# Performance work log

Hardware: AMD Instinct MI355X
Metric: run time of the kernel (lower is better)

Reference implementation:

```python
import jax, jax.numpy as jnp
import numpy as np

N_NODES = 50000
N_EDGES = 500000
IN_DIM = 128
H1, C1 = 4, 64   # layer1: heads=4, out=64, concat -> 256
H2, C2 = 1, 64   # layer2: heads=1, out=64


def setup_inputs() -> dict:
    key = jax.random.key(0)
    ks = jax.random.split(key, 16)
    p = lambda k, shp: (jax.random.normal(k, shp, dtype=jnp.float32) * 0.1)
    return {
        "x": jax.random.normal(ks[0], (N_NODES, IN_DIM), dtype=jnp.float32),
        "edge_index": jax.random.randint(ks[1], (2, N_EDGES), 0, N_NODES, dtype=jnp.int32),
        "edge_attr": jax.random.uniform(ks[2], (N_EDGES, 1), dtype=jnp.float32),
        # layer 1 params
        "W1": p(ks[3], (IN_DIM, H1 * C1)),
        "We1": p(ks[4], (1, H1 * C1)),
        "as1": p(ks[5], (H1, C1)),
        "ad1": p(ks[6], (H1, C1)),
        "ae1": p(ks[7], (H1, C1)),
        "b1": jnp.zeros((H1 * C1,), dtype=jnp.float32),
        # layer 2 params
        "W2": p(ks[8], (H1 * C1, H2 * C2)),
        "We2": p(ks[9], (1, H2 * C2)),
        "as2": p(ks[10], (H2, C2)),
        "ad2": p(ks[11], (H2, C2)),
        "ae2": p(ks[12], (H2, C2)),
        "b2": jnp.zeros((H2 * C2,), dtype=jnp.float32),
    }


def _add_self_loops(src, dst, edge_attr, n):
    # PyG fill_value='mean': loop edge_attr = mean of incoming edge attrs per node
    cnt = jax.ops.segment_sum(jnp.ones((src.shape[0],), edge_attr.dtype), dst, num_segments=n)
    loop_attr = jax.ops.segment_sum(edge_attr, dst, num_segments=n) / jnp.maximum(cnt, 1.0)[:, None]
    idx = jnp.arange(n, dtype=src.dtype)
    return (jnp.concatenate([src, idx]), jnp.concatenate([dst, idx]),
            jnp.concatenate([edge_attr, loop_attr], axis=0))


def _gat_conv(x, src, dst, edge_attr, W, We, a_src, a_dst, a_edge, bias, heads, out_ch):
    n = x.shape[0]
    h = (x @ W).reshape(n, heads, out_ch)                      # [N,H,C]
    e = (edge_attr @ We).reshape(-1, heads, out_ch)            # [E,H,C]
    alpha = ((h * a_src).sum(-1)[src]                          # gather src score
             + (h * a_dst).sum(-1)[dst]                        # gather dst score
             + (e * a_edge).sum(-1))                           # [E,H]
    alpha = jax.nn.leaky_relu(alpha, 0.2)
    m = jax.ops.segment_max(alpha, dst, num_segments=n)        # per-target max
    alpha = jnp.exp(alpha - m[dst])
    denom = jax.ops.segment_sum(alpha, dst, num_segments=n)
    alpha = alpha / (denom[dst] + 1e-16)
    out = jax.ops.segment_sum(h[src] * alpha[..., None], dst, num_segments=n)
    return out.reshape(n, heads * out_ch) + bias


def reference(x, edge_index, edge_attr, W1, We1, as1, ad1, ae1, b1,
              W2, We2, as2, ad2, ae2, b2):
    src, dst = edge_index[0], edge_index[1]
    src, dst, ea = _add_self_loops(src, dst, edge_attr, x.shape[0])
    h = jax.nn.elu(_gat_conv(x, src, dst, ea, W1, We1, as1, ad1, ae1, b1, H1, C1))
    return _gat_conv(h, src, dst, ea, W2, We2, as2, ad2, ae2, b2, H2, C2)
```

## Files before the change

### kernel.cpp

```cpp
#include <hip/hip_runtime.h>
#include <math.h>

#define NN 50000
#define NE 500000
#define DIM 128
#define HC1 256
#define HC2 64
#define RSTR 64
#define CAPM 63
#define EPB 1024
#define NBUCKET ((NE + EPB - 1) / EPB)
#define GB ((NN + 63) / 64)

typedef __attribute__((ext_vector_type(8))) short short8;
typedef __attribute__((ext_vector_type(4))) float floatx4;


__device__ __forceinline__ unsigned short f2bf(float f) {
  unsigned int u = __float_as_uint(f);
  unsigned int r = (u + 0x7FFFu + ((u >> 16) & 1u)) >> 16;
  return (unsigned short)r;
}
__device__ __forceinline__ float bf2f(unsigned short s) {
  return __uint_as_float(((unsigned int)s) << 16);
}

__device__ __forceinline__ float waveReduce(float v) {
  v += __shfl_down(v, 32);
  v += __shfl_down(v, 16);
  v += __shfl_down(v, 8);
  v += __shfl_down(v, 4);
  v += __shfl_down(v, 2);
  v += __shfl_down(v, 1);
  return v;
}


__global__ __launch_bounds__(256) void k_prep(const float* __restrict__ W1,
                                              const float* __restrict__ W2,
                                              const float* __restrict__ We1,
                                              const float* __restrict__ ae1,
                                              const float* __restrict__ We2,
                                              const float* __restrict__ ae2,
                                              unsigned short* __restrict__ W1T,
                                              unsigned short* __restrict__ W2T,
                                              float* __restrict__ ce) {
  int b = blockIdx.x, t = threadIdx.x;
  if (b < 128) {
    int idx = b * 256 + t;
    int n = idx >> 7, k = idx & 127;
    W1T[idx] = f2bf(W1[k * 256 + n]);
  } else if (b < 192) {
    int idx = (b - 128) * 256 + t;
    int n = idx >> 8, k = idx & 255;
    W2T[idx] = f2bf(W2[k * 64 + n]);
  } else {
    int h = t >> 6, lane = t & 63;
    float p = We1[h * 64 + lane] * ae1[h * 64 + lane];
    p = waveReduce(p);
    if (lane == 0) ce[h] = p;
    if (h == 0) {
      float q = We2[lane] * ae2[lane];
      q = waveReduce(q);
      if (lane == 0) ce[4] = q;
    }
  }
}


__global__ __launch_bounds__(256) void k_bucket(const int* __restrict__ src,
                                                const int* __restrict__ dst,
                                                const float* __restrict__ ea,
                                                unsigned int* __restrict__ ebuf) {
  int t = threadIdx.x;
  int e0 = blockIdx.x * EPB + t;
  int dv[4]; float ev[4]; unsigned int sv[4]; bool ok[4];
#pragma unroll
  for (int k = 0; k < 4; k++) {
    int e = e0 + k * 256;
    ok[k] = (e < NE);
    int ee = ok[k] ? e : 0;
    dv[k] = dst[ee];
    ev[k] = ea[ee];
    sv[k] = (unsigned int)src[ee];
  }
  unsigned int old[4];
#pragma unroll
  for (int k = 0; k < 4; k++) {
    if (ok[k]) old[k] = atomicAdd(&ebuf[(unsigned long long)dv[k] * RSTR], 1u);
  }
#pragma unroll
  for (int k = 0; k < 4; k++) {
    if (ok[k] && old[k] < CAPM) {
      unsigned int ea16 = __float2uint_rn(ev[k] * 65536.0f);
      if (ea16 > 65535u) ea16 = 65535u;
      ebuf[(unsigned long long)dv[k] * RSTR + 1 + old[k]] = (ea16 << 16) | sv[k];
    }
  }
}


__global__ __launch_bounds__(256) void k_gemm1(const float* __restrict__ x,
                                               const unsigned short* __restrict__ W1T,
                                               const float* __restrict__ as1,
                                               const float* __restrict__ ad1,
                                               unsigned short* __restrict__ h1b,
                                               float* __restrict__ ss1,
                                               float* __restrict__ sd1) {
  __shared__ unsigned short As[64 * 136];
  int t = threadIdx.x;
  int wave = t >> 6, lane = t & 63;
  int q = lane >> 4, ln = lane & 15;
  int m0 = blockIdx.x * 64;
  int n0 = wave * 64;

  short8 bfr[4][4];
#pragma unroll
  for (int c = 0; c < 4; c++)
#pragma unroll
    for (int ks = 0; ks < 4; ks++)
      bfr[c][ks] = *(const short8*)&W1T[(n0 + ln * 4 + c) * 128 + ks * 32 + q * 8];

#pragma unroll
  for (int rep = 0; rep < 8; rep++) {
    int chunk = t + 256 * rep;
    int m = chunk >> 5, kk = (chunk & 31) * 4;
    int gr = m0 + m;
    float4 v = (gr < NN) ? *(const float4*)&x[gr * DIM + kk]
                         : make_float4(0.f, 0.f, 0.f, 0.f);
    ushort4 o;
    o.x = f2bf(v.x); o.y = f2bf(v.y); o.z = f2bf(v.z); o.w = f2bf(v.w);
    *(ushort4*)&As[m * 136 + kk] = o;
  }
  __syncthreads();

  floatx4 acc[4][4];
#pragma unroll
  for (int r = 0; r < 4; r++)
#pragma unroll
    for (int c = 0; c < 4; c++) acc[r][c] = (floatx4){0.f, 0.f, 0.f, 0.f};

#pragma unroll
  for (int ks = 0; ks < 4; ks++) {
    short8 afr[4];
#pragma unroll
    for (int r = 0; r < 4; r++)
      afr[r] = *(const short8*)&As[(r * 16 + ln) * 136 + ks * 32 + q * 8];
#pragma unroll
    for (int r = 0; r < 4; r++)
#pragma unroll
      for (int c = 0; c < 4; c++)
        acc[r][c] = __builtin_amdgcn_mfma_f32_16x16x32_bf16(afr[r], bfr[c][ks], acc[r][c], 0, 0, 0);
  }

  float4 a4 = *(const float4*)&as1[n0 + ln * 4];
  float4 d4 = *(const float4*)&ad1[n0 + ln * 4];

#pragma unroll
  for (int r = 0; r < 4; r++) {
#pragma unroll
    for (int i = 0; i < 4; i++) {
      int gm = m0 + r * 16 + q * 4 + i;
      if (gm < NN) {
        ushort4 o;
        o.x = f2bf(acc[r][0][i]);
        o.y = f2bf(acc[r][1][i]);
        o.z = f2bf(acc[r][2][i]);
        o.w = f2bf(acc[r][3][i]);
        *(ushort4*)&h1b[gm * HC1 + n0 + ln * 4] = o;
      }
      float ps = acc[r][0][i] * a4.x;
      float pd = acc[r][0][i] * d4.x;
      ps = fmaf(acc[r][1][i], a4.y, ps);
      pd = fmaf(acc[r][1][i], d4.y, pd);
      ps = fmaf(acc[r][2][i], a4.z, ps);
      pd = fmaf(acc[r][2][i], d4.z, pd);
      ps = fmaf(acc[r][3][i], a4.w, ps);
      pd = fmaf(acc[r][3][i], d4.w, pd);
#pragma unroll
      for (int m = 1; m < 16; m <<= 1) {
        ps += __shfl_xor(ps, m);
        pd += __shfl_xor(pd, m);
      }
      if (ln == 0 && gm < NN) {
        ss1[gm * 4 + wave] = ps;
        sd1[gm * 4 + wave] = pd;
      }
    }
  }
}

__global__ __launch_bounds__(256) void k_gemm2m(const unsigned short* __restrict__ out1b,
                                                const unsigned short* __restrict__ W2T,
                                                const float* __restrict__ as2,
                                                const float* __restrict__ ad2,
                                                unsigned short* __restrict__ h2b,
                                                float* __restrict__ ss2,
                                                float* __restrict__ sd2) {
  __shared__ unsigned short As[64 * 264];
  __shared__ float ssp[4][64], sdp[4][64];
  int t = threadIdx.x;
  int wave = t >> 6, lane = t & 63;
  int q = lane >> 4, ln = lane & 15;
  int m0 = blockIdx.x * 64;
  int n0 = wave * 16;

  short8 bfr[8];
#pragma unroll
  for (int ks = 0; ks < 8; ks++)
    bfr[ks] = *(const short8*)&W2T[(n0 + ln) * 256 + ks * 32 + q * 8];

  short8 zero8 = {0, 0, 0, 0, 0, 0, 0, 0};
#pragma unroll
  for (int rep = 0; rep < 8; rep++) {
    int chunk = t + 256 * rep;
    int m = chunk >> 5, kk = (chunk & 31) * 8;
    int gr = m0 + m;
    short8 vv = (gr < NN) ? *(const short8*)&out1b[gr * 256 + kk] : zero8;
    *(short8*)&As[m * 264 + kk] = vv;
  }
  __syncthreads();

  floatx4 acc[4];
#pragma unroll
  for (int r = 0; r < 4; r++) acc[r] = (floatx4){0.f, 0.f, 0.f, 0.f};

#pragma unroll
  for (int ks = 0; ks < 8; ks++) {
#pragma unroll
    for (int r = 0; r < 4; r++) {
      short8 afr = *(const short8*)&As[(r * 16 + ln) * 264 + ks * 32 + q * 8];
      acc[r] = __builtin_amdgcn_mfma_f32_16x16x32_bf16(afr, bfr[ks], acc[r], 0, 0, 0);
    }
  }

  float as2v = as2[n0 + ln], ad2v = ad2[n0 + ln];
#pragma unroll
  for (int r = 0; r < 4; r++) {
#pragma unroll
    for (int i = 0; i < 4; i++) {
      int gm = m0 + r * 16 + q * 4 + i;
      if (gm < NN) h2b[gm * HC2 + n0 + ln] = f2bf(acc[r][i]);
      float ps = acc[r][i] * as2v;
      float pd = acc[r][i] * ad2v;
#pragma unroll
      for (int m = 1; m < 16; m <<= 1) {
        ps += __shfl_xor(ps, m);
        pd += __shfl_xor(pd, m);
      }
      if (ln == 0) {
        ssp[wave][r * 16 + q * 4 + i] = ps;
        sdp[wave][r * 16 + q * 4 + i] = pd;
      }
    }
  }
  __syncthreads();
  if (t < 64) {
    int gm = m0 + t;
    if (gm < NN) {
      ss2[gm] = ssp[0][t] + ssp[1][t] + ssp[2][t] + ssp[3][t];
      sd2[gm] = sdp[0][t] + sdp[1][t] + sdp[2][t] + sdp[3][t];
    }
  }
}


__global__ __launch_bounds__(256) void k_agg1(const unsigned short* __restrict__ h1b,
                                              const unsigned int* __restrict__ ebuf,
                                              const float* __restrict__ ss1,
                                              const float* __restrict__ sd1,
                                              const float* __restrict__ ce,
                                              const float* __restrict__ b1,
                                              unsigned short* __restrict__ out1b) {
  int v = (blockIdx.x * blockDim.x + threadIdx.x) >> 6;
  int lane = threadIdx.x & 63;
  int h = lane >> 4;
  int c4 = lane * 4;
  int l16 = lane & 15;
  int vu = __builtin_amdgcn_readfirstlane(v);
  unsigned int craw = ebuf[(unsigned long long)vu * RSTR];
  int cn = (craw < CAPM) ? (int)craw : CAPM;
  cn = __builtin_amdgcn_readfirstlane(cn);
  int beg1 = vu * RSTR + 1;
  int end1 = beg1 + cn;
  float sdh = sd1[vu * 4 + h];
  float ceh = ce[h];
  float4 acc = make_float4(0.f, 0.f, 0.f, 0.f);
  float l = 0.f;
  float easum = 0.f;

  for (int base = beg1; base < end1; base += 16) {
    unsigned int meta = ebuf[base + l16];
#pragma unroll
    for (int half = 0; half < 2; half++) {
      if (base + half * 8 >= end1) break;
      float ssv[8], ea8[8];
      ushort4 u[8];
      bool vld[8];
#pragma unroll
      for (int jj = 0; jj < 8; jj++) {
        int j = half * 8 + jj;
        bool val = (base + j < end1);
        unsigned int m = __builtin_amdgcn_readlane(meta, j);
        int sj = val ? (int)(m & 0xFFFFu) : 0;
        ea8[jj] = (float)(m >> 16) * (1.0f / 65536.0f);
        vld[jj] = val;
        ssv[jj] = ss1[sj * 4 + h];
        u[jj] = *(const ushort4*)&h1b[sj * HC1 + c4];
      }
#pragma unroll
      for (int jj = 0; jj < 8; jj++) {
        easum += vld[jj] ? ea8[jj] : 0.f;
        float xx = fmaf(ea8[jj], ceh, ssv[jj] + sdh);
        xx = fmaxf(xx, 0.2f * xx);
        float a = vld[jj] ? __expf(xx) : 0.f;
        l += a;
        acc.x = fmaf(a, bf2f(u[jj].x), acc.x);
        acc.y = fmaf(a, bf2f(u[jj].y), acc.y);
        acc.z = fmaf(a, bf2f(u[jj].z), acc.z);
        acc.w = fmaf(a, bf2f(u[jj].w), acc.w);
      }
    }
  }
  {
    float lea = easum / fmaxf((float)cn, 1.0f);
    float xx = fmaf(lea, ceh, ss1[vu * 4 + h] + sdh);
    xx = fmaxf(xx, 0.2f * xx);
    float a = __expf(xx);
    ushort4 u = *(const ushort4*)&h1b[vu * HC1 + c4];
    l += a;
    acc.x = fmaf(a, bf2f(u.x), acc.x);
    acc.y = fmaf(a, bf2f(u.y), acc.y);
    acc.z = fmaf(a, bf2f(u.z), acc.z);
    acc.w = fmaf(a, bf2f(u.w), acc.w);
  }
  float inv = 1.f / (l + 1e-16f);
  float4 bv = *(const float4*)&b1[c4];
  float4 o;
  o.x = acc.x * inv + bv.x;
  o.y = acc.y * inv + bv.y;
  o.z = acc.z * inv + bv.z;
  o.w = acc.w * inv + bv.w;
  o.x = (o.x > 0.f) ? o.x : expm1f(o.x);
  o.y = (o.y > 0.f) ? o.y : expm1f(o.y);
  o.z = (o.z > 0.f) ? o.z : expm1f(o.z);
  o.w = (o.w > 0.f) ? o.w : expm1f(o.w);
  ushort4 ob;
  ob.x = f2bf(o.x); ob.y = f2bf(o.y); ob.z = f2bf(o.z); ob.w = f2bf(o.w);
  *(ushort4*)&out1b[vu * HC1 + c4] = ob;
}

__global__ __launch_bounds__(256) void k_agg2(const unsigned short* __restrict__ h2b,
                                              const unsigned int* __restrict__ ebuf,
                                              const float* __restrict__ ss2,
                                              const float* __restrict__ sd2,
                                              const float* __restrict__ ce,
                                              const float* __restrict__ b2,
                                              float* __restrict__ out) {
  int v = (blockIdx.x * blockDim.x + threadIdx.x) >> 6;
  int lane = threadIdx.x & 63;
  int g = lane >> 4;
  int c = lane & 15;
  int l16 = lane & 15;
  int vu = __builtin_amdgcn_readfirstlane(v);
  unsigned int craw = ebuf[(unsigned long long)vu * RSTR];
  int cn = (craw < CAPM) ? (int)craw : CAPM;
  cn = __builtin_amdgcn_readfirstlane(cn);
  int beg1 = vu * RSTR + 1;
  int end1 = beg1 + cn;
  float sdv = sd2[vu];
  float cev = ce[4];
  float4 acc = make_float4(0.f, 0.f, 0.f, 0.f);
  float l = 0.f;
  float easum = 0.f;

  for (int base = beg1; base < end1; base += 16) {
    int nb = end1 - base;
    unsigned int meta = ebuf[base + l16];
    float ssv[4], eav[4];
    bool vld[4];
    ushort4 u[4];
#pragma unroll
    for (int sub = 0; sub < 4; sub++) {
      int j = sub * 4 + g;
      bool val = (j < nb);
      unsigned int m = (unsigned int)__shfl((int)meta, j);
      int sj = val ? (int)(m & 0xFFFFu) : 0;
      eav[sub] = (float)(m >> 16) * (1.0f / 65536.0f);
      vld[sub] = val;
      ssv[sub] = ss2[sj];
      u[sub] = *(const ushort4*)&h2b[sj * HC2 + c * 4];
    }
#pragma unroll
    for (int sub = 0; sub < 4; sub++) {
      easum += vld[sub] ? eav[sub] : 0.f;
      float xx = fmaf(eav[sub], cev, ssv[sub] + sdv);
      xx = fmaxf(xx, 0.2f * xx);
      float a = vld[sub] ? __expf(xx) : 0.f;
      l += a;
      acc.x = fmaf(a, bf2f(u[sub].x), acc.x);
      acc.y = fmaf(a, bf2f(u[sub].y), acc.y);
      acc.z = fmaf(a, bf2f(u[sub].z), acc.z);
      acc.w = fmaf(a, bf2f(u[sub].w), acc.w);
    }
  }
#pragma unroll
  for (int m = 16; m <= 32; m <<= 1) {
    acc.x += __shfl_xor(acc.x, m);
    acc.y += __shfl_xor(acc.y, m);
    acc.z += __shfl_xor(acc.z, m);
    acc.w += __shfl_xor(acc.w, m);
    l += __shfl_xor(l, m);
    easum += __shfl_xor(easum, m);
  }
  {
    float lea = easum / fmaxf((float)cn, 1.0f);
    float xx = fmaf(lea, cev, ss2[vu] + sdv);
    xx = fmaxf(xx, 0.2f * xx);
    float a = __expf(xx);
    ushort4 us = *(const ushort4*)&h2b[vu * HC2 + c * 4];
    l += a;
    acc.x = fmaf(a, bf2f(us.x), acc.x);
    acc.y = fmaf(a, bf2f(us.y), acc.y);
    acc.z = fmaf(a, bf2f(us.z), acc.z);
    acc.w = fmaf(a, bf2f(us.w), acc.w);
  }
  if (g == 0) {
    float inv = 1.f / (l + 1e-16f);
    float4 bv = *(const float4*)&b2[c * 4];
    float4 o;
    o.x = acc.x * inv + bv.x;
    o.y = acc.y * inv + bv.y;
    o.z = acc.z * inv + bv.z;
    o.w = acc.w * inv + bv.w;
    *(float4*)&out[vu * HC2 + c * 4] = o;
  }
}


extern "C" void kernel_launch(void* const* d_in, const int* in_sizes, int n_in,
                              void* d_out, int out_size, void* d_ws, size_t ws_size,
                              hipStream_t stream) {
  const float* x   = (const float*)d_in[0];
  const int*   ei  = (const int*)d_in[1];
  const float* ea  = (const float*)d_in[2];
  const float* W1  = (const float*)d_in[3];
  const float* We1 = (const float*)d_in[4];
  const float* as1 = (const float*)d_in[5];
  const float* ad1 = (const float*)d_in[6];
  const float* ae1 = (const float*)d_in[7];
  const float* b1  = (const float*)d_in[8];
  const float* W2  = (const float*)d_in[9];
  const float* We2 = (const float*)d_in[10];
  const float* as2 = (const float*)d_in[11];
  const float* ad2 = (const float*)d_in[12];
  const float* ae2 = (const float*)d_in[13];
  const float* b2  = (const float*)d_in[14];
  const int* srcp = ei;
  const int* dstp = ei + NE;

  char* w = (char*)d_ws;
  float* ce      = (float*)(w + 3200064);
  float* ss1     = (float*)(w + 3200640);
  float* sd1     = (float*)(w + 4000640);
  float* ss2     = (float*)(w + 4800640);
  float* sd2     = (float*)(w + 5000640);
  unsigned int* ebuf = (unsigned int*)(w + 5200640);
  unsigned short* h1b   = (unsigned short*)(w + 18000640);
  unsigned short* out1b = (unsigned short*)(w + 43600640);
  unsigned short* h2b   = (unsigned short*)(w + 69200640);
  unsigned short* W1T   = (unsigned short*)(w + 75600640);
  unsigned short* W2T   = (unsigned short*)(w + 75666176);

  hipMemsetAsync(w + 5200640, 0, 12800000, stream);

  k_prep<<<193, 256, 0, stream>>>(W1, W2, We1, ae1, We2, ae2, W1T, W2T, ce);
  k_bucket<<<NBUCKET, 256, 0, stream>>>(srcp, dstp, ea, ebuf);
  k_gemm1<<<GB, 256, 0, stream>>>(x, W1T, as1, ad1, h1b, ss1, sd1);

  k_agg1<<<(NN * 64 + 255) / 256, 256, 0, stream>>>(h1b, ebuf, ss1, sd1, ce, b1, out1b);

  k_gemm2m<<<(NN + 63) / 64, 256, 0, stream>>>(out1b, W2T, as2, ad2, h2b, ss2, sd2);
  k_agg2<<<(NN * 64 + 255) / 256, 256, 0, stream>>>(h2b, ebuf, ss2, sd2, ce, b2,
                                                    (float*)d_out);
}
```

Before: 229.9 us.

## Split layer-1 aggregation across channel slices and edge groups; drop ebuf memset

Layer-1 aggregation now uses 8 blocks per group of 4 nodes, one per 32-channel slice. Within each wave, 8 lane groups each take a different edge and their partial sums are combined with cross-lane shuffles. This replaces the serial per-node loop over all edges with readlane broadcasts. The attention scores ss1/sd1 are stored head-major so the per-head gathers are contiguous. The full 12.8MB memset of the edge buffer is replaced by zeroing only the per-node count words inside k_prep. The cost is 8x more blocks, and the per-node metadata and score loads are repeated in every slice.

```diff
diff --git a/kernel.cpp b/kernel.cpp
--- a/kernel.cpp
+++ b/kernel.cpp
@@ -11,6 +11,7 @@
 #define EPB 1024
 #define NBUCKET ((NE + EPB - 1) / EPB)
 #define GB ((NN + 63) / 64)
+#define NSS 50048
 
 typedef __attribute__((ext_vector_type(8))) short short8;
 typedef __attribute__((ext_vector_type(4))) float floatx4;
@@ -44,7 +45,8 @@
                                               const float* __restrict__ ae2,
                                               unsigned short* __restrict__ W1T,
                                               unsigned short* __restrict__ W2T,
-                                              float* __restrict__ ce) {
+                                              float* __restrict__ ce,
+                                              unsigned int* __restrict__ ebuf) {
   int b = blockIdx.x, t = threadIdx.x;
   if (b < 128) {
     int idx = b * 256 + t;
@@ -54,7 +56,7 @@
     int idx = (b - 128) * 256 + t;
     int n = idx >> 8, k = idx & 255;
     W2T[idx] = f2bf(W2[k * 64 + n]);
-  } else {
+  } else if (b == 192) {
     int h = t >> 6, lane = t & 63;
     float p = We1[h * 64 + lane] * ae1[h * 64 + lane];
     p = waveReduce(p);
@@ -64,6 +66,9 @@
       q = waveReduce(q);
       if (lane == 0) ce[4] = q;
     }
+  } else {
+    int idx = (b - 193) * 256 + t;
+    if (idx < NN) ebuf[(unsigned long long)idx * RSTR] = 0u;
   }
 }
 
@@ -183,8 +188,8 @@
         pd += __shfl_xor(pd, m);
       }
       if (ln == 0 && gm < NN) {
-        ss1[gm * 4 + wave] = ps;
-        sd1[gm * 4 + wave] = pd;
+        ss1[wave * NSS + gm] = ps;
+        sd1[wave * NSS + gm] = pd;
       }
     }
   }
@@ -272,62 +277,59 @@
                                               const float* __restrict__ ce,
                                               const float* __restrict__ b1,
                                               unsigned short* __restrict__ out1b) {
-  int v = (blockIdx.x * blockDim.x + threadIdx.x) >> 6;
+  int slice = blockIdx.x & 7;
+  int wave = threadIdx.x >> 6;
   int lane = threadIdx.x & 63;
-  int h = lane >> 4;
-  int c4 = lane * 4;
-  int l16 = lane & 15;
-  int vu = __builtin_amdgcn_readfirstlane(v);
+  int vu = (blockIdx.x >> 3) * 4 + wave;
+  if (vu >= NN) return;
+  int g = lane >> 3;
+  int cl = lane & 7;
+  int h = slice >> 1;
+  int cbase = slice * 32 + cl * 4;
+
   unsigned int craw = ebuf[(unsigned long long)vu * RSTR];
   int cn = (craw < CAPM) ? (int)craw : CAPM;
-  cn = __builtin_amdgcn_readfirstlane(cn);
   int beg1 = vu * RSTR + 1;
-  int end1 = beg1 + cn;
-  float sdh = sd1[vu * 4 + h];
+  float sdh = sd1[h * NSS + vu];
   float ceh = ce[h];
   float4 acc = make_float4(0.f, 0.f, 0.f, 0.f);
   float l = 0.f;
   float easum = 0.f;
 
-  for (int base = beg1; base < end1; base += 16) {
-    unsigned int meta = ebuf[base + l16];
-#pragma unroll
-    for (int half = 0; half < 2; half++) {
-      if (base + half * 8 >= end1) break;
-      float ssv[8], ea8[8];
-      ushort4 u[8];
-      bool vld[8];
-#pragma unroll
-      for (int jj = 0; jj < 8; jj++) {
-        int j = half * 8 + jj;
-        bool val = (base + j < end1);
-        unsigned int m = __builtin_amdgcn_readlane(meta, j);
-        int sj = val ? (int)(m & 0xFFFFu) : 0;
-        ea8[jj] = (float)(m >> 16) * (1.0f / 65536.0f);
-        vld[jj] = val;
-        ssv[jj] = ss1[sj * 4 + h];
-        u[jj] = *(const ushort4*)&h1b[sj * HC1 + c4];
-      }
-#pragma unroll
-      for (int jj = 0; jj < 8; jj++) {
-        easum += vld[jj] ? ea8[jj] : 0.f;
-        float xx = fmaf(ea8[jj], ceh, ssv[jj] + sdh);
-        xx = fmaxf(xx, 0.2f * xx);
-        float a = vld[jj] ? __expf(xx) : 0.f;
-        l += a;
-        acc.x = fmaf(a, bf2f(u[jj].x), acc.x);
-        acc.y = fmaf(a, bf2f(u[jj].y), acc.y);
-        acc.z = fmaf(a, bf2f(u[jj].z), acc.z);
-        acc.w = fmaf(a, bf2f(u[jj].w), acc.w);
-      }
-    }
+  for (int j0 = 0; j0 < cn; j0 += 8) {
+    int j = j0 + g;
+    bool val = (j < cn);
+    int jc = val ? j : 0;
+    unsigned int m = ebuf[beg1 + jc];
+    int sj = (int)(m & 0xFFFFu);
+    float eav = (float)(m >> 16) * (1.0f / 65536.0f);
+    float ssv = ss1[h * NSS + sj];
+    ushort4 u = *(const ushort4*)&h1b[sj * HC1 + cbase];
+    float xx = fmaf(eav, ceh, ssv + sdh);
+    xx = fmaxf(xx, 0.2f * xx);
+    float a = val ? __expf(xx) : 0.f;
+    l += a;
+    easum += val ? eav : 0.f;
+    acc.x = fmaf(a, bf2f(u.x), acc.x);
+    acc.y = fmaf(a, bf2f(u.y), acc.y);
+    acc.z = fmaf(a, bf2f(u.z), acc.z);
+    acc.w = fmaf(a, bf2f(u.w), acc.w);
+  }
+#pragma unroll
+  for (int m = 8; m <= 32; m <<= 1) {
+    acc.x += __shfl_xor(acc.x, m);
+    acc.y += __shfl_xor(acc.y, m);
+    acc.z += __shfl_xor(acc.z, m);
+    acc.w += __shfl_xor(acc.w, m);
+    l += __shfl_xor(l, m);
+    easum += __shfl_xor(easum, m);
   }
   {
     float lea = easum / fmaxf((float)cn, 1.0f);
-    float xx = fmaf(lea, ceh, ss1[vu * 4 + h] + sdh);
+    float xx = fmaf(lea, ceh, ss1[h * NSS + vu] + sdh);
     xx = fmaxf(xx, 0.2f * xx);
     float a = __expf(xx);
-    ushort4 u = *(const ushort4*)&h1b[vu * HC1 + c4];
+    ushort4 u = *(const ushort4*)&h1b[vu * HC1 + cbase];
     l += a;
     acc.x = fmaf(a, bf2f(u.x), acc.x);
     acc.y = fmaf(a, bf2f(u.y), acc.y);
@@ -335,7 +337,7 @@
     acc.w = fmaf(a, bf2f(u.w), acc.w);
   }
   float inv = 1.f / (l + 1e-16f);
-  float4 bv = *(const float4*)&b1[c4];
+  float4 bv = *(const float4*)&b1[cbase];
   float4 o;
   o.x = acc.x * inv + bv.x;
   o.y = acc.y * inv + bv.y;
@@ -345,9 +347,11 @@
   o.y = (o.y > 0.f) ? o.y : expm1f(o.y);
   o.z = (o.z > 0.f) ? o.z : expm1f(o.z);
   o.w = (o.w > 0.f) ? o.w : expm1f(o.w);
-  ushort4 ob;
-  ob.x = f2bf(o.x); ob.y = f2bf(o.y); ob.z = f2bf(o.z); ob.w = f2bf(o.w);
-  *(ushort4*)&out1b[vu * HC1 + c4] = ob;
+  if (g == 0) {
+    ushort4 ob;
+    ob.x = f2bf(o.x); ob.y = f2bf(o.y); ob.z = f2bf(o.z); ob.w = f2bf(o.w);
+    *(ushort4*)&out1b[vu * HC1 + cbase] = ob;
+  }
 }
 
 __global__ __launch_bounds__(256) void k_agg2(const unsigned short* __restrict__ h2b,
@@ -460,25 +464,23 @@
   const int* dstp = ei + NE;
 
   char* w = (char*)d_ws;
-  float* ce      = (float*)(w + 3200064);
-  float* ss1     = (float*)(w + 3200640);
-  float* sd1     = (float*)(w + 4000640);
-  float* ss2     = (float*)(w + 4800640);
-  float* sd2     = (float*)(w + 5000640);
-  unsigned int* ebuf = (unsigned int*)(w + 5200640);
-  unsigned short* h1b   = (unsigned short*)(w + 18000640);
-  unsigned short* out1b = (unsigned short*)(w + 43600640);
-  unsigned short* h2b   = (unsigned short*)(w + 69200640);
-  unsigned short* W1T   = (unsigned short*)(w + 75600640);
-  unsigned short* W2T   = (unsigned short*)(w + 75666176);
-
-  hipMemsetAsync(w + 5200640, 0, 12800000, stream);
-
-  k_prep<<<193, 256, 0, stream>>>(W1, W2, We1, ae1, We2, ae2, W1T, W2T, ce);
+  float* ce      = (float*)(w + 0);
+  float* ss1     = (float*)(w + 1024);
+  float* sd1     = (float*)(w + 801792);
+  float* ss2     = (float*)(w + 1602560);
+  float* sd2     = (float*)(w + 1802560);
+  unsigned int* ebuf = (unsigned int*)(w + 2002944);
+  unsigned short* h1b   = (unsigned short*)(w + 14802944);
+  unsigned short* out1b = (unsigned short*)(w + 40402944);
+  unsigned short* h2b   = (unsigned short*)(w + 66002944);
+  unsigned short* W1T   = (unsigned short*)(w + 72402944);
+  unsigned short* W2T   = (unsigned short*)(w + 72468480);
+
+  k_prep<<<389, 256, 0, stream>>>(W1, W2, We1, ae1, We2, ae2, W1T, W2T, ce, ebuf);
   k_bucket<<<NBUCKET, 256, 0, stream>>>(srcp, dstp, ea, ebuf);
   k_gemm1<<<GB, 256, 0, stream>>>(x, W1T, as1, ad1, h1b, ss1, sd1);
 
-  k_agg1<<<(NN * 64 + 255) / 256, 256, 0, stream>>>(h1b, ebuf, ss1, sd1, ce, b1, out1b);
+  k_agg1<<<8 * ((NN + 3) / 4), 256, 0, stream>>>(h1b, ebuf, ss1, sd1, ce, b1, out1b);
 
   k_gemm2m<<<(NN + 63) / 64, 256, 0, stream>>>(out1b, W2T, as2, ad2, h2b, ss2, sd2);
   k_agg2<<<(NN * 64 + 255) / 256, 256, 0, stream>>>(h2b, ebuf, ss2, sd2, ce, b2,
```

Result: slower. 336.7 us (+46.4%).

## Fuse bucketing with GEMM1, aggregation1 with GEMM2, drop memset

Applied to the files above, without the earlier changes.

Replaces the 12.8MB workspace memset by zeroing only the per-node counters inside the prep kernel. Bucketing and the first GEMM now run as one launch, split by block index. Layer-1 aggregation is fused with the second GEMM: each 1024-thread block aggregates 64 nodes into shared memory and runs the MFMA on them directly, so the out1b global round-trip and two launches go away. In exchange the aggregation now processes only 4 edges per batch instead of 8, which may expose more gather latency. The large 1024-thread blocks may also reduce occupancy.

```diff
diff --git a/kernel.cpp b/kernel.cpp
--- a/kernel.cpp
+++ b/kernel.cpp
@@ -44,7 +44,8 @@
                                               const float* __restrict__ ae2,
                                               unsigned short* __restrict__ W1T,
                                               unsigned short* __restrict__ W2T,
-                                              float* __restrict__ ce) {
+                                              float* __restrict__ ce,
+                                              unsigned int* __restrict__ ebuf) {
   int b = blockIdx.x, t = threadIdx.x;
   if (b < 128) {
     int idx = b * 256 + t;
@@ -54,7 +55,7 @@
     int idx = (b - 128) * 256 + t;
     int n = idx >> 8, k = idx & 255;
     W2T[idx] = f2bf(W2[k * 64 + n]);
-  } else {
+  } else if (b == 192) {
     int h = t >> 6, lane = t & 63;
     float p = We1[h * 64 + lane] * ae1[h * 64 + lane];
     p = waveReduce(p);
@@ -64,43 +65,18 @@
       q = waveReduce(q);
       if (lane == 0) ce[4] = q;
     }
-  }
-}
-
-
-__global__ __launch_bounds__(256) void k_bucket(const int* __restrict__ src,
-                                                const int* __restrict__ dst,
-                                                const float* __restrict__ ea,
-                                                unsigned int* __restrict__ ebuf) {
-  int t = threadIdx.x;
-  int e0 = blockIdx.x * EPB + t;
-  int dv[4]; float ev[4]; unsigned int sv[4]; bool ok[4];
-#pragma unroll
-  for (int k = 0; k < 4; k++) {
-    int e = e0 + k * 256;
-    ok[k] = (e < NE);
-    int ee = ok[k] ? e : 0;
-    dv[k] = dst[ee];
-    ev[k] = ea[ee];
-    sv[k] = (unsigned int)src[ee];
-  }
-  unsigned int old[4];
-#pragma unroll
-  for (int k = 0; k < 4; k++) {
-    if (ok[k]) old[k] = atomicAdd(&ebuf[(unsigned long long)dv[k] * RSTR], 1u);
-  }
-#pragma unroll
-  for (int k = 0; k < 4; k++) {
-    if (ok[k] && old[k] < CAPM) {
-      unsigned int ea16 = __float2uint_rn(ev[k] * 65536.0f);
-      if (ea16 > 65535u) ea16 = 65535u;
-      ebuf[(unsigned long long)dv[k] * RSTR + 1 + old[k]] = (ea16 << 16) | sv[k];
-    }
-  }
-}
-
-
-__global__ __launch_bounds__(256) void k_gemm1(const float* __restrict__ x,
+  } else {
+    int idx = (b - 193) * 256 + t;
+    if (idx < NN) ebuf[(unsigned long long)idx * RSTR] = 0u;
+  }
+}
+
+
+__global__ __launch_bounds__(256) void k_fused(const int* __restrict__ src,
+                                               const int* __restrict__ dst,
+                                               const float* __restrict__ ea,
+                                               unsigned int* __restrict__ ebuf,
+                                               const float* __restrict__ x,
                                                const unsigned short* __restrict__ W1T,
                                                const float* __restrict__ as1,
                                                const float* __restrict__ ad1,
@@ -109,9 +85,38 @@
                                                float* __restrict__ sd1) {
   __shared__ unsigned short As[64 * 136];
   int t = threadIdx.x;
+
+  if (blockIdx.x < NBUCKET) {
+    int e0 = blockIdx.x * EPB + t;
+    int dv[4]; float ev[4]; unsigned int sv[4]; bool ok[4];
+#pragma unroll
+    for (int k = 0; k < 4; k++) {
+      int e = e0 + k * 256;
+      ok[k] = (e < NE);
+      int ee = ok[k] ? e : 0;
+      dv[k] = dst[ee];
+      ev[k] = ea[ee];
+      sv[k] = (unsigned int)src[ee];
+    }
+    unsigned int old[4];
+#pragma unroll
+    for (int k = 0; k < 4; k++) {
+      if (ok[k]) old[k] = atomicAdd(&ebuf[(unsigned long long)dv[k] * RSTR], 1u);
+    }
+#pragma unroll
+    for (int k = 0; k < 4; k++) {
+      if (ok[k] && old[k] < CAPM) {
+        unsigned int ea16 = __float2uint_rn(ev[k] * 65536.0f);
+        if (ea16 > 65535u) ea16 = 65535u;
+        ebuf[(unsigned long long)dv[k] * RSTR + 1 + old[k]] = (ea16 << 16) | sv[k];
+      }
+    }
+    return;
+  }
+
   int wave = t >> 6, lane = t & 63;
   int q = lane >> 4, ln = lane & 15;
-  int m0 = blockIdx.x * 64;
+  int m0 = (blockIdx.x - NBUCKET) * 64;
   int n0 = wave * 64;
 
   short8 bfr[4][4];
@@ -190,67 +195,143 @@
   }
 }
 
-__global__ __launch_bounds__(256) void k_gemm2m(const unsigned short* __restrict__ out1b,
-                                                const unsigned short* __restrict__ W2T,
-                                                const float* __restrict__ as2,
-                                                const float* __restrict__ ad2,
-                                                unsigned short* __restrict__ h2b,
-                                                float* __restrict__ ss2,
-                                                float* __restrict__ sd2) {
-  __shared__ unsigned short As[64 * 264];
+
+__global__ __launch_bounds__(1024) void k_agg1g2(const unsigned short* __restrict__ h1b,
+                                                 const unsigned int* __restrict__ ebuf,
+                                                 const float* __restrict__ ss1,
+                                                 const float* __restrict__ sd1,
+                                                 const float* __restrict__ ce,
+                                                 const float* __restrict__ b1,
+                                                 const unsigned short* __restrict__ W2T,
+                                                 const float* __restrict__ as2,
+                                                 const float* __restrict__ ad2,
+                                                 unsigned short* __restrict__ h2b,
+                                                 float* __restrict__ ss2,
+                                                 float* __restrict__ sd2) {
+  __shared__ unsigned short Ao[64 * 264];
   __shared__ float ssp[4][64], sdp[4][64];
   int t = threadIdx.x;
   int wave = t >> 6, lane = t & 63;
-  int q = lane >> 4, ln = lane & 15;
   int m0 = blockIdx.x * 64;
-  int n0 = wave * 16;
-
-  short8 bfr[8];
-#pragma unroll
-  for (int ks = 0; ks < 8; ks++)
-    bfr[ks] = *(const short8*)&W2T[(n0 + ln) * 256 + ks * 32 + q * 8];
-
-  short8 zero8 = {0, 0, 0, 0, 0, 0, 0, 0};
-#pragma unroll
-  for (int rep = 0; rep < 8; rep++) {
-    int chunk = t + 256 * rep;
-    int m = chunk >> 5, kk = (chunk & 31) * 8;
-    int gr = m0 + m;
-    short8 vv = (gr < NN) ? *(const short8*)&out1b[gr * 256 + kk] : zero8;
-    *(short8*)&As[m * 264 + kk] = vv;
+
+  {
+    int h = lane >> 4;
+    int c4 = lane * 4;
+    int l16 = lane & 15;
+    float ceh = ce[h];
+    float4 bv = *(const float4*)&b1[c4];
+
+    for (int nd = 0; nd < 4; nd++) {
+      int vu = m0 + wave * 4 + nd;
+      int lrow = wave * 4 + nd;
+      if (vu >= NN) {
+        ushort4 z = {0, 0, 0, 0};
+        *(ushort4*)&Ao[lrow * 264 + c4] = z;
+        continue;
+      }
+      unsigned int craw = ebuf[(unsigned long long)vu * RSTR];
+      int cn = (craw < CAPM) ? (int)craw : CAPM;
+      cn = __builtin_amdgcn_readfirstlane(cn);
+      int beg1 = vu * RSTR + 1;
+      int end1 = beg1 + cn;
+      float sdh = sd1[vu * 4 + h];
+      float4 acc = make_float4(0.f, 0.f, 0.f, 0.f);
+      float l = 0.f;
+      float easum = 0.f;
+
+      for (int base = beg1; base < end1; base += 16) {
+        unsigned int meta = ebuf[base + l16];
+#pragma unroll
+        for (int b4 = 0; b4 < 4; b4++) {
+          if (base + b4 * 4 >= end1) break;
+          float ssv[4], ea4[4];
+          ushort4 u[4];
+          bool vld[4];
+#pragma unroll
+          for (int jj = 0; jj < 4; jj++) {
+            int j = b4 * 4 + jj;
+            bool val = (base + j < end1);
+            unsigned int m = __builtin_amdgcn_readlane(meta, j);
+            int sj = val ? (int)(m & 0xFFFFu) : 0;
+            ea4[jj] = (float)(m >> 16) * (1.0f / 65536.0f);
+            vld[jj] = val;
+            ssv[jj] = ss1[sj * 4 + h];
+            u[jj] = *(const ushort4*)&h1b[sj * HC1 + c4];
+          }
+#pragma unroll
+          for (int jj = 0; jj < 4; jj++) {
+            easum += vld[jj] ? ea4[jj] : 0.f;
+            float xx = fmaf(ea4[jj], ceh, ssv[jj] + sdh);
+            xx = fmaxf(xx, 0.2f * xx);
+            float a = vld[jj] ? __expf(xx) : 0.f;
+            l += a;
+            acc.x = fmaf(a, bf2f(u[jj].x), acc.x);
+            acc.y = fmaf(a, bf2f(u[jj].y), acc.y);
+            acc.z = fmaf(a, bf2f(u[jj].z), acc.z);
+            acc.w = fmaf(a, bf2f(u[jj].w), acc.w);
+          }
+        }
+      }
+      {
+        float lea = easum / fmaxf((float)cn, 1.0f);
+        float xx = fmaf(lea, ceh, ss1[vu * 4 + h] + sdh);
+        xx = fmaxf(xx, 0.2f * xx);
+        float a = __expf(xx);
+        ushort4 u = *(const ushort4*)&h1b[vu * HC1 + c4];
+        l += a;
+        acc.x = fmaf(a, bf2f(u.x), acc.x);
+        acc.y = fmaf(a, bf2f(u.y), acc.y);
+        acc.z = fmaf(a, bf2f(u.z), acc.z);
+        acc.w = fmaf(a, bf2f(u.w), acc.w);
+      }
+      float inv = 1.f / (l + 1e-16f);
+      float4 o;
+      o.x = acc.x * inv + bv.x;
+      o.y = acc.y * inv + bv.y;
+      o.z = acc.z * inv + bv.z;
+      o.w = acc.w * inv + bv.w;
+      o.x = (o.x > 0.f) ? o.x : expm1f(o.x);
+      o.y = (o.y > 0.f) ? o.y : expm1f(o.y);
+      o.z = (o.z > 0.f) ? o.z : expm1f(o.z);
+      o.w = (o.w > 0.f) ? o.w : expm1f(o.w);
+      ushort4 ob;
+      ob.x = f2bf(o.x); ob.y = f2bf(o.y); ob.z = f2bf(o.z); ob.w = f2bf(o.w);
+      *(ushort4*)&Ao[lrow * 264 + c4] = ob;
+    }
   }
   __syncthreads();
 
-  floatx4 acc[4];
-#pragma unroll
-  for (int r = 0; r < 4; r++) acc[r] = (floatx4){0.f, 0.f, 0.f, 0.f};
-
-#pragma unroll
-  for (int ks = 0; ks < 8; ks++) {
-#pragma unroll
-    for (int r = 0; r < 4; r++) {
-      short8 afr = *(const short8*)&As[(r * 16 + ln) * 264 + ks * 32 + q * 8];
-      acc[r] = __builtin_amdgcn_mfma_f32_16x16x32_bf16(afr, bfr[ks], acc[r], 0, 0, 0);
-    }
-  }
-
-  float as2v = as2[n0 + ln], ad2v = ad2[n0 + ln];
-#pragma unroll
-  for (int r = 0; r < 4; r++) {
+  {
+    int q = lane >> 4, ln = lane & 15;
+    int r = wave >> 2, c = wave & 3;
+
+    short8 bfr[8];
+#pragma unroll
+    for (int ks = 0; ks < 8; ks++)
+      bfr[ks] = *(const short8*)&W2T[(c * 16 + ln) * 256 + ks * 32 + q * 8];
+
+    floatx4 acc = (floatx4){0.f, 0.f, 0.f, 0.f};
+#pragma unroll
+    for (int ks = 0; ks < 8; ks++) {
+      short8 afr = *(const short8*)&Ao[(r * 16 + ln) * 264 + ks * 32 + q * 8];
+      acc = __builtin_amdgcn_mfma_f32_16x16x32_bf16(afr, bfr[ks], acc, 0, 0, 0);
+    }
+
+    float as2v = as2[c * 16 + ln], ad2v = ad2[c * 16 + ln];
 #pragma unroll
     for (int i = 0; i < 4; i++) {
       int gm = m0 + r * 16 + q * 4 + i;
-      if (gm < NN) h2b[gm * HC2 + n0 + ln] = f2bf(acc[r][i]);
-      float ps = acc[r][i] * as2v;
-      float pd = acc[r][i] * ad2v;
+      if (gm < NN) h2b[gm * HC2 + c * 16 + ln] = f2bf(acc[i]);
+      float ps = acc[i] * as2v;
+      float pd = acc[i] * ad2v;
 #pragma unroll
       for (int m = 1; m < 16; m <<= 1) {
         ps += __shfl_xor(ps, m);
         pd += __shfl_xor(pd, m);
       }
       if (ln == 0) {
-        ssp[wave][r * 16 + q * 4 + i] = ps;
-        sdp[wave][r * 16 + q * 4 + i] = pd;
+        ssp[c][r * 16 + q * 4 + i] = ps;
+        sdp[c][r * 16 + q * 4 + i] = pd;
       }
     }
   }
@@ -262,92 +343,6 @@
       sd2[gm] = sdp[0][t] + sdp[1][t] + sdp[2][t] + sdp[3][t];
     }
   }
-}
-
-
-__global__ __launch_bounds__(256) void k_agg1(const unsigned short* __restrict__ h1b,
-                                              const unsigned int* __restrict__ ebuf,
-                                              const float* __restrict__ ss1,
-                                              const float* __restrict__ sd1,
-                                              const float* __restrict__ ce,
-                                              const float* __restrict__ b1,
-                                              unsigned short* __restrict__ out1b) {
-  int v = (blockIdx.x * blockDim.x + threadIdx.x) >> 6;
-  int lane = threadIdx.x & 63;
-  int h = lane >> 4;
-  int c4 = lane * 4;
-  int l16 = lane & 15;
-  int vu = __builtin_amdgcn_readfirstlane(v);
-  unsigned int craw = ebuf[(unsigned long long)vu * RSTR];
-  int cn = (craw < CAPM) ? (int)craw : CAPM;
-  cn = __builtin_amdgcn_readfirstlane(cn);
-  int beg1 = vu * RSTR + 1;
-  int end1 = beg1 + cn;
-  float sdh = sd1[vu * 4 + h];
-  float ceh = ce[h];
-  float4 acc = make_float4(0.f, 0.f, 0.f, 0.f);
-  float l = 0.f;
-  float easum = 0.f;
-
-  for (int base = beg1; base < end1; base += 16) {
-    unsigned int meta = ebuf[base + l16];
-#pragma unroll
-    for (int half = 0; half < 2; half++) {
-      if (base + half * 8 >= end1) break;
-      float ssv[8], ea8[8];
-      ushort4 u[8];
-      bool vld[8];
-#pragma unroll
-      for (int jj = 0; jj < 8; jj++) {
-        int j = half * 8 + jj;
-        bool val = (base + j < end1);
-        unsigned int m = __builtin_amdgcn_readlane(meta, j);
-        int sj = val ? (int)(m & 0xFFFFu) : 0;
-        ea8[jj] = (float)(m >> 16) * (1.0f / 65536.0f);
-        vld[jj] = val;
-        ssv[jj] = ss1[sj * 4 + h];
-        u[jj] = *(const ushort4*)&h1b[sj * HC1 + c4];
-      }
-#pragma unroll
-      for (int jj = 0; jj < 8; jj++) {
-        easum += vld[jj] ? ea8[jj] : 0.f;
-        float xx = fmaf(ea8[jj], ceh, ssv[jj] + sdh);
-        xx = fmaxf(xx, 0.2f * xx);
-        float a = vld[jj] ? __expf(xx) : 0.f;
-        l += a;
-        acc.x = fmaf(a, bf2f(u[jj].x), acc.x);
-        acc.y = fmaf(a, bf2f(u[jj].y), acc.y);
-        acc.z = fmaf(a, bf2f(u[jj].z), acc.z);
-        acc.w = fmaf(a, bf2f(u[jj].w), acc.w);
-      }
-    }
-  }
-  {
-    float lea = easum / fmaxf((float)cn, 1.0f);
-    float xx = fmaf(lea, ceh, ss1[vu * 4 + h] + sdh);
-    xx = fmaxf(xx, 0.2f * xx);
-    float a = __expf(xx);
-    ushort4 u = *(const ushort4*)&h1b[vu * HC1 + c4];
-    l += a;
-    acc.x = fmaf(a, bf2f(u.x), acc.x);
-    acc.y = fmaf(a, bf2f(u.y), acc.y);
-    acc.z = fmaf(a, bf2f(u.z), acc.z);
-    acc.w = fmaf(a, bf2f(u.w), acc.w);
-  }
-  float inv = 1.f / (l + 1e-16f);
-  float4 bv = *(const float4*)&b1[c4];
-  float4 o;
-  o.x = acc.x * inv + bv.x;
-  o.y = acc.y * inv + bv.y;
-  o.z = acc.z * inv + bv.z;
-  o.w = acc.w * inv + bv.w;
-  o.x = (o.x > 0.f) ? o.x : expm1f(o.x);
-  o.y = (o.y > 0.f) ? o.y : expm1f(o.y);
-  o.z = (o.z > 0.f) ? o.z : expm1f(o.z);
-  o.w = (o.w > 0.f) ? o.w : expm1f(o.w);
-  ushort4 ob;
-  ob.x = f2bf(o.x); ob.y = f2bf(o.y); ob.z = f2bf(o.z); ob.w = f2bf(o.w);
-  *(ushort4*)&out1b[vu * HC1 + c4] = ob;
 }
 
 __global__ __launch_bounds__(256) void k_agg2(const unsigned short* __restrict__ h2b,
@@ -460,27 +455,24 @@
   const int* dstp = ei + NE;
 
   char* w = (char*)d_ws;
-  float* ce      = (float*)(w + 3200064);
-  float* ss1     = (float*)(w + 3200640);
-  float* sd1     = (float*)(w + 4000640);
-  float* ss2     = (float*)(w + 4800640);
-  float* sd2     = (float*)(w + 5000640);
-  unsigned int* ebuf = (unsigned int*)(w + 5200640);
-  unsigned short* h1b   = (unsigned short*)(w + 18000640);
-  unsigned short* out1b = (unsigned short*)(w + 43600640);
-  unsigned short* h2b   = (unsigned short*)(w + 69200640);
-  unsigned short* W1T   = (unsigned short*)(w + 75600640);
-  unsigned short* W2T   = (unsigned short*)(w + 75666176);
-
-  hipMemsetAsync(w + 5200640, 0, 12800000, stream);
-
-  k_prep<<<193, 256, 0, stream>>>(W1, W2, We1, ae1, We2, ae2, W1T, W2T, ce);
-  k_bucket<<<NBUCKET, 256, 0, stream>>>(srcp, dstp, ea, ebuf);
-  k_gemm1<<<GB, 256, 0, stream>>>(x, W1T, as1, ad1, h1b, ss1, sd1);
-
-  k_agg1<<<(NN * 64 + 255) / 256, 256, 0, stream>>>(h1b, ebuf, ss1, sd1, ce, b1, out1b);
-
-  k_gemm2m<<<(NN + 63) / 64, 256, 0, stream>>>(out1b, W2T, as2, ad2, h2b, ss2, sd2);
+  float* ce      = (float*)(w + 0);
+  float* ss1     = (float*)(w + 1024);
+  float* sd1     = (float*)(w + 801024);
+  float* ss2     = (float*)(w + 1601024);
+  float* sd2     = (float*)(w + 1801024);
+  unsigned int* ebuf = (unsigned int*)(w + 2001024);
+  unsigned short* h1b = (unsigned short*)(w + 14801024);
+  unsigned short* h2b = (unsigned short*)(w + 40401024);
+  unsigned short* W1T = (unsigned short*)(w + 46801024);
+  unsigned short* W2T = (unsigned short*)(w + 46866560);
+
+  k_prep<<<389, 256, 0, stream>>>(W1, W2, We1, ae1, We2, ae2, W1T, W2T, ce, ebuf);
+  k_fused<<<NBUCKET + GB, 256, 0, stream>>>(srcp, dstp, ea, ebuf,
+                                            x, W1T, as1, ad1, h1b, ss1, sd1);
+
+  k_agg1g2<<<GB, 1024, 0, stream>>>(h1b, ebuf, ss1, sd1, ce, b1,
+                                    W2T, as2, ad2, h2b, ss2, sd2);
+
   k_agg2<<<(NN * 64 + 255) / 256, 256, 0, stream>>>(h2b, ebuf, ss2, sd2, ce, b2,
                                                     (float*)d_out);
 }
```

Result: no change. 229.4 us (-0.2%).
